# Kernel optimization log

Measured on AMD Instinct MI355X. Metric: run time of the kernel, lower is better.

Reference implementation:

```python
import jax, jax.numpy as jnp
import numpy as np

# Constants from the torch module
S_DECAY = 0.95    # sentence_decay
P_DECAY = 0.99    # paragraph_decay
D_DECAY = 0.999   # document_decay
ALPHA = 0.1       # delta_update alpha for sentence/paragraph
DOC_ALPHA = 0.05  # delta_update alpha for document
BETA = 1.0
PARA_GROUP = 5    # sentences per paragraph
EPS = 1e-12       # F.normalize eps


def _normalize(x):
    # matches torch.nn.functional.normalize(x, dim=-1)
    return x / jnp.maximum(jnp.linalg.norm(x, axis=-1, keepdims=True), EPS)


def _delta_step(M, kn, v, alpha, beta):
    # M: [H, dk, dv]; kn: [dk] (already L2-normalized); v: [dv]
    # M_new = M @ (I - alpha * kn kn^T) + beta * kn v^T   (erase matrix is symmetric,
    # so the einsum 'hkv,hkj->hjv' form equals this rank-1 update -- no dk x dk matrix needed)
    kTM = jnp.einsum('k,hkv->hv', kn, M)                       # [H, dv]
    return M - alpha * kn[None, :, None] * kTM[:, None, :] \
             + beta * (kn[:, None] * v[None, :])[None, :, :]


def _scan_updates(M0, K, V, decay, alpha, beta):
    # Streaming delta-rule: per step, decay then erase/write.
    def step(M, kv):
        k, v = kv
        M = M * decay
        M = _delta_step(M, _normalize(k), v, alpha, beta)
        return M, None
    M, _ = jax.lax.scan(step, M0, (K, V))
    return M


def setup_inputs() -> dict:
    key = jax.random.key(0)
    ks = jax.random.split(key, 7)
    T, d_emb, d_k, d_v, H = 1000, 768, 256, 256, 8
    emb = jax.random.normal(ks[0], (T, d_emb), dtype=jnp.float32)
    q = jax.random.normal(ks[1], (d_k,), dtype=jnp.float32)
    W_k = jax.random.normal(ks[2], (d_emb, d_k), dtype=jnp.float32) * 0.02
    b_k = jax.random.normal(ks[3], (d_k,), dtype=jnp.float32) * 0.02
    W_v = jax.random.normal(ks[4], (d_emb, d_v), dtype=jnp.float32) * 0.02
    b_v = jax.random.normal(ks[5], (d_v,), dtype=jnp.float32) * 0.02
    M_sent0 = jnp.zeros((H, d_k, d_v), dtype=jnp.float32)
    M_para0 = jnp.zeros((H, d_k, d_v), dtype=jnp.float32)
    M_doc0 = jnp.zeros((H, d_k, d_v), dtype=jnp.float32)
    return {"emb": emb, "q": q, "W_k": W_k, "b_k": b_k, "W_v": W_v, "b_v": b_v,
            "M_sent0": M_sent0, "M_para0": M_para0, "M_doc0": M_doc0}


def reference(emb, q, W_k, b_k, W_v, b_v, M_sent0, M_para0, M_doc0):
    T, d_emb = emb.shape
    # Level 1: sentence memory -- one delta update per sentence embedding
    K = emb @ W_k + b_k            # [T, dk]
    V = emb @ W_v + b_v            # [T, dv]
    M_sent = _scan_updates(M_sent0, K, V, S_DECAY, ALPHA, BETA)
    # Level 2: paragraph memory -- mean of each group of 5 sentence embeddings
    para_emb = emb.reshape(T // PARA_GROUP, PARA_GROUP, d_emb).mean(axis=1)
    PK = para_emb @ W_k + b_k
    PV = para_emb @ W_v + b_v
    M_para = _scan_updates(M_para0, PK, PV, P_DECAY, ALPHA, BETA)
    # Level 3: document memory -- single update from paragraph-memory statistics
    doc_k = M_para.mean(axis=0).mean(axis=-1)   # [dk]
    doc_v = M_para.mean(axis=0).mean(axis=0)    # [dv]
    M_doc = M_doc0 * D_DECAY
    M_doc = _delta_step(M_doc, _normalize(doc_k), doc_v, DOC_ALPHA, BETA)
    # recall(q, level='all')
    qn = _normalize(q)
    def recall(M):
        return jnp.einsum('hkv,k->hv', M, qn).mean(axis=0)   # [dv]
    return 0.2 * recall(M_sent) + 0.3 * recall(M_para) + 0.5 * recall(M_doc)
```

## Files before the change

### kernel.cpp

```cpp
#include <hip/hip_runtime.h>
#include <hip/hip_bf16.h>

#define ALPHA   0.1f
#define S_DECAY 0.95f
#define P_DECAY 0.99f
#define D_EMB   768
#define DK      256

template<int ctrl, int row_mask>
__device__ __forceinline__ float dpp_add(float x) {
    int y = __builtin_amdgcn_update_dpp(0, __float_as_int(x), ctrl, row_mask, 0xF, true);
    return x + __int_as_float(y);
}

template<int N>
__device__ __forceinline__ void wave_allred_arr(float (&x)[N]) {
#pragma unroll
    for (int n = 0; n < N; ++n) x[n] = dpp_add<0xB1,  0xF>(x[n]);
#pragma unroll
    for (int n = 0; n < N; ++n) x[n] = dpp_add<0x4E,  0xF>(x[n]);
#pragma unroll
    for (int n = 0; n < N; ++n) x[n] = dpp_add<0x141, 0xF>(x[n]);
#pragma unroll
    for (int n = 0; n < N; ++n) x[n] = dpp_add<0x140, 0xF>(x[n]);
#pragma unroll
    for (int n = 0; n < N; ++n) x[n] = dpp_add<0x142, 0xA>(x[n]);
#pragma unroll
    for (int n = 0; n < N; ++n) x[n] = dpp_add<0x143, 0xC>(x[n]);
#pragma unroll
    for (int n = 0; n < N; ++n)
        x[n] = __int_as_float(__builtin_amdgcn_readlane(__float_as_int(x[n]), 63));
}

__device__ __forceinline__ float dot4v(const float4& a, const float4& b) {
    float t0 = a.x * b.x; t0 = fmaf(a.y, b.y, t0);
    float t1 = a.z * b.z; t1 = fmaf(a.w, b.w, t1);
    return t0 + t1;
}

__device__ __forceinline__ float rl(float x, int lane) {
    return __int_as_float(__builtin_amdgcn_readlane(__float_as_int(x), lane));
}

__global__ __launch_bounds__(256) void prep_kernel(
    const float* __restrict__ emb,
    const float* __restrict__ Wk, const float* __restrict__ bk,
    const float* __restrict__ Wv, const float* __restrict__ bv,
    float* __restrict__ K, float* __restrict__ V, float* __restrict__ USrev,
    float* __restrict__ out, int T)
{
    const int tid = threadIdx.x;
    const int bid = blockIdx.x;
    const int NBLK = (T / 4) * 2;
    if (bid >= NBLK) {
        const int PADS = ((T + 63) / 64) * 64;
        for (int i = tid; i < (PADS - T) * DK; i += 256) USrev[(size_t)T * DK + i] = 0.f;
        out[tid] = 0.f;
        return;
    }
    const int mat = bid & 1;
    const int r0  = (bid >> 1) * 4;

    __shared__ float se[4][D_EMB];
    __shared__ float s_red[4][4];

    const float4* emb4 = reinterpret_cast<const float4*>(emb);
#pragma unroll
    for (int r = 0; r < 4; ++r) {
        if (tid < D_EMB / 4)
            reinterpret_cast<float4*>(se[r])[tid] = emb4[(size_t)(r0 + r) * (D_EMB / 4) + tid];
    }
    __syncthreads();

    const float* Wp = mat ? Wv : Wk;
    const float* bp = mat ? bv : bk;
    const int j = tid;

    float a0 = 0.f, a1 = 0.f, a2 = 0.f, a3 = 0.f;
    float c0 = Wp[j],        c1 = Wp[j + DK],     c2 = Wp[j + 2*DK], c3 = Wp[j + 3*DK];
    float p0 = Wp[j + 4*DK], p1 = Wp[j + 5*DK],   p2 = Wp[j + 6*DK], p3 = Wp[j + 7*DK];

    for (int d = 0; d < D_EMB; d += 4) {
        int dn = d + 8; if (dn >= D_EMB) dn = 0;
        const float* wn = Wp + (size_t)dn * DK + j;
        float n0 = wn[0], n1 = wn[DK], n2 = wn[2*DK], n3 = wn[3*DK];

        float4 e0 = *reinterpret_cast<const float4*>(&se[0][d]);
        float4 e1 = *reinterpret_cast<const float4*>(&se[1][d]);
        float4 e2 = *reinterpret_cast<const float4*>(&se[2][d]);
        float4 e3 = *reinterpret_cast<const float4*>(&se[3][d]);

        a0 = fmaf(e0.x, c0, a0); a0 = fmaf(e0.y, c1, a0);
        a0 = fmaf(e0.z, c2, a0); a0 = fmaf(e0.w, c3, a0);
        a1 = fmaf(e1.x, c0, a1); a1 = fmaf(e1.y, c1, a1);
        a1 = fmaf(e1.z, c2, a1); a1 = fmaf(e1.w, c3, a1);
        a2 = fmaf(e2.x, c0, a2); a2 = fmaf(e2.y, c1, a2);
        a2 = fmaf(e2.z, c2, a2); a2 = fmaf(e2.w, c3, a2);
        a3 = fmaf(e3.x, c0, a3); a3 = fmaf(e3.y, c1, a3);
        a3 = fmaf(e3.z, c2, a3); a3 = fmaf(e3.w, c3, a3);

        c0 = p0; c1 = p1; c2 = p2; c3 = p3;
        p0 = n0; p1 = n1; p2 = n2; p3 = n3;
    }

    float bj = bp[j];
    float o0 = a0 + bj, o1 = a1 + bj, o2 = a2 + bj, o3 = a3 + bj;
    float* dst = mat ? V : K;
    dst[(size_t)(r0 + 0) * DK + j] = o0;
    dst[(size_t)(r0 + 1) * DK + j] = o1;
    dst[(size_t)(r0 + 2) * DK + j] = o2;
    dst[(size_t)(r0 + 3) * DK + j] = o3;

    if (mat == 0) {
        const int wave = tid >> 6, l = tid & 63;
        float red[4] = { o0*o0, o1*o1, o2*o2, o3*o3 };
        wave_allred_arr(red);
        if (l == 0) {
            s_red[wave][0] = red[0]; s_red[wave][1] = red[1];
            s_red[wave][2] = red[2]; s_red[wave][3] = red[3];
        }
        __syncthreads();
        float t0 = s_red[0][0] + s_red[1][0] + s_red[2][0] + s_red[3][0];
        float t1 = s_red[0][1] + s_red[1][1] + s_red[2][1] + s_red[3][1];
        float t2 = s_red[0][2] + s_red[1][2] + s_red[2][2] + s_red[3][2];
        float t3 = s_red[0][3] + s_red[1][3] + s_red[2][3] + s_red[3][3];
        USrev[(size_t)(T - 1 - (r0 + 0)) * DK + j] = o0 * (1.0f / fmaxf(sqrtf(t0), 1e-12f));
        USrev[(size_t)(T - 1 - (r0 + 1)) * DK + j] = o1 * (1.0f / fmaxf(sqrtf(t1), 1e-12f));
        USrev[(size_t)(T - 1 - (r0 + 2)) * DK + j] = o2 * (1.0f / fmaxf(sqrtf(t2), 1e-12f));
        USrev[(size_t)(T - 1 - (r0 + 3)) * DK + j] = o3 * (1.0f / fmaxf(sqrtf(t3), 1e-12f));
    }
}

#define SU_STRIDE 260
__global__ __launch_bounds__(256) void graminv_kernel(
    const float* __restrict__ K, const float* __restrict__ V,
    const float* __restrict__ USrev,
    float* __restrict__ UPrev, float* __restrict__ UPfwd,
    float* __restrict__ PV, float* __restrict__ SVv,
    float* __restrict__ AinvT, float* __restrict__ F1, float* __restrict__ biasF,
    int P, int NCS, int NCP)
{
    __shared__ float sU[64 * SU_STRIDE];
    __shared__ float sA[64 * 65];
    __shared__ float sX[64 * 65];
    __shared__ float s_sv[64];
    __shared__ float s_pd[64];
    __shared__ float4 s_f1w[4][64];
    const int tid = threadIdx.x, wv = tid >> 6, l = tid & 63;
    const int bid = blockIdx.x;
    int type, m;
    if (bid < NCS)            { type = 0; m = bid; }
    else if (bid < NCS + NCP) { type = 1; m = bid - NCS; }
    else                      { type = 2; m = bid - NCS - NCP; }

    if (tid < 64) s_pd[tid] = powf(P_DECAY, (float)tid);

    float4 f1p = make_float4(0.f, 0.f, 0.f, 0.f);

    if (type == 0) {
        const float4* U4 = reinterpret_cast<const float4*>(USrev) + (size_t)m * 4096;
        for (int idx = tid; idx < 4096; idx += 256) {
            float4 t = U4[idx];
            int row = idx >> 6, c4 = (idx & 63) << 2;
            *reinterpret_cast<float4*>(&sU[row * SU_STRIDE + c4]) = t;
        }
    } else if (type == 1) {
        const float4* K4 = reinterpret_cast<const float4*>(K);
        for (int ii = 0; ii < 16; ++ii) {
            int i = wv * 16 + ii;
            int p = P - 1 - (64 * m + i);
            float4 u = make_float4(0.f, 0.f, 0.f, 0.f);
            if (p >= 0) {
                float4 pk = make_float4(0.f, 0.f, 0.f, 0.f);
#pragma unroll
                for (int s = 0; s < 5; ++s) {
                    float4 k4 = K4[(size_t)(5 * p + s) * 64 + l];
                    pk.x += k4.x; pk.y += k4.y; pk.z += k4.z; pk.w += k4.w;
                }
                pk.x *= 0.2f; pk.y *= 0.2f; pk.z *= 0.2f; pk.w *= 0.2f;
                float red[1] = { dot4v(pk, pk) };
                wave_allred_arr(red);
                float inv = 1.0f / fmaxf(sqrtf(red[0]), 1e-12f);
                u = make_float4(pk.x * inv, pk.y * inv, pk.z * inv, pk.w * inv);
            }
            *reinterpret_cast<float4*>(&sU[i * SU_STRIDE + 4 * l]) = u;
            reinterpret_cast<float4*>(UPrev)[(size_t)(64 * m + i) * 64 + l] = u;
        }
    } else {
        const float4* K4 = reinterpret_cast<const float4*>(K);
        const float4* V4 = reinterpret_cast<const float4*>(V);
        for (int ii = 0; ii < 16; ++ii) {
            int i = wv * 16 + ii;
            int p = 64 * m + i;
            float4 u = make_float4(0.f, 0.f, 0.f, 0.f);
            float sv = 0.f;
            if (p < P) {
                float4 pk = make_float4(0.f, 0.f, 0.f, 0.f);
                float4 pv = make_float4(0.f, 0.f, 0.f, 0.f);
#pragma unroll
                for (int s = 0; s < 5; ++s) {
                    float4 k4 = K4[(size_t)(5 * p + s) * 64 + l];
                    float4 v4 = V4[(size_t)(5 * p + s) * 64 + l];
                    pk.x += k4.x; pk.y += k4.y; pk.z += k4.z; pk.w += k4.w;
                    pv.x += v4.x; pv.y += v4.y; pv.z += v4.z; pv.w += v4.w;
                }
                pk.x *= 0.2f; pk.y *= 0.2f; pk.z *= 0.2f; pk.w *= 0.2f;
                pv.x *= 0.2f; pv.y *= 0.2f; pv.z *= 0.2f; pv.w *= 0.2f;
                reinterpret_cast<float4*>(PV)[(size_t)p * 64 + l] = pv;
                float red[2] = { dot4v(pk, pk), pv.x + pv.y + pv.z + pv.w };
                wave_allred_arr(red);
                float inv = 1.0f / fmaxf(sqrtf(red[0]), 1e-12f);
                u = make_float4(pk.x * inv, pk.y * inv, pk.z * inv, pk.w * inv);
                sv = red[1];
            }
            *reinterpret_cast<float4*>(&sU[i * SU_STRIDE + 4 * l]) = u;
            reinterpret_cast<float4*>(UPfwd)[(size_t)(64 * m + i) * 64 + l] = u;
            if (l == 0) { s_sv[i] = sv; SVv[64 * m + i] = sv; }
            float f = powf(P_DECAY, (float)(63 - i)) * sv;
            f1p.x = fmaf(f, u.x, f1p.x); f1p.y = fmaf(f, u.y, f1p.y);
            f1p.z = fmaf(f, u.z, f1p.z); f1p.w = fmaf(f, u.w, f1p.w);
        }
        s_f1w[wv][l] = f1p;
    }
    __syncthreads();

    if (type == 2 && wv == 0) {
        float4 a = s_f1w[0][l], b = s_f1w[1][l], c = s_f1w[2][l], d = s_f1w[3][l];
        float4 tot = make_float4(a.x+b.x+c.x+d.x, a.y+b.y+c.y+d.y,
                                 a.z+b.z+c.z+d.z, a.w+b.w+c.w+d.w);
        reinterpret_cast<float4*>(F1)[(size_t)m * 64 + l] = tot;
    }

    const int tr = tid & 15, tcg = tid >> 4;
    const int i0 = tr * 4, j0 = tcg * 4;
    if (tcg <= tr) {
        float g[4][4];
#pragma unroll
        for (int r = 0; r < 4; ++r)
#pragma unroll
            for (int c = 0; c < 4; ++c) g[r][c] = 0.f;
        for (int k4 = 0; k4 < 64; ++k4) {
            float4 A0 = *reinterpret_cast<const float4*>(&sU[(i0    ) * SU_STRIDE + 4*k4]);
            float4 A1 = *reinterpret_cast<const float4*>(&sU[(i0 + 1) * SU_STRIDE + 4*k4]);
            float4 A2 = *reinterpret_cast<const float4*>(&sU[(i0 + 2) * SU_STRIDE + 4*k4]);
            float4 A3 = *reinterpret_cast<const float4*>(&sU[(i0 + 3) * SU_STRIDE + 4*k4]);
            float4 B0 = *reinterpret_cast<const float4*>(&sU[(j0    ) * SU_STRIDE + 4*k4]);
            float4 B1 = *reinterpret_cast<const float4*>(&sU[(j0 + 1) * SU_STRIDE + 4*k4]);
            float4 B2 = *reinterpret_cast<const float4*>(&sU[(j0 + 2) * SU_STRIDE + 4*k4]);
            float4 B3 = *reinterpret_cast<const float4*>(&sU[(j0 + 3) * SU_STRIDE + 4*k4]);
            g[0][0] += dot4v(A0, B0); g[0][1] += dot4v(A0, B1);
            g[0][2] += dot4v(A0, B2); g[0][3] += dot4v(A0, B3);
            g[1][0] += dot4v(A1, B0); g[1][1] += dot4v(A1, B1);
            g[1][2] += dot4v(A1, B2); g[1][3] += dot4v(A1, B3);
            g[2][0] += dot4v(A2, B0); g[2][1] += dot4v(A2, B1);
            g[2][2] += dot4v(A2, B2); g[2][3] += dot4v(A2, B3);
            g[3][0] += dot4v(A3, B0); g[3][1] += dot4v(A3, B1);
            g[3][2] += dot4v(A3, B2); g[3][3] += dot4v(A3, B3);
        }
#pragma unroll
        for (int r = 0; r < 4; ++r)
#pragma unroll
            for (int c = 0; c < 4; ++c) {
                int gi = i0 + r, gj = j0 + c;
                float val = 0.f;
                if (gj < gi) {
                    val = ALPHA * g[r][c];
                    if (type == 2) val *= s_pd[gi - gj];
                }
                sA[gi * 65 + gj] = val;
            }
    } else {
#pragma unroll
        for (int r = 0; r < 4; ++r)
#pragma unroll
            for (int c = 0; c < 4; ++c)
                sA[(i0 + r) * 65 + j0 + c] = 0.f;
    }
    __syncthreads();

    if (type == 2 && wv == 0) {
        float dotb = 0.f;
#pragma unroll
        for (int jj = 0; jj < 64; ++jj)
            dotb = fmaf(sA[l * 65 + jj], s_sv[jj], dotb);
        biasF[m * 64 + l] = dotb * (1.0f / ALPHA);
    }

    {
        const int base = wv * 16;
        float x[16];
#pragma unroll
        for (int r = 0; r < 16; ++r) x[r] = (base + r == l) ? 1.f : 0.f;
        for (int s = 0; s < 4; ++s) {
            if (wv == s) {
#pragma unroll
                for (int i = 1; i < 16; ++i)
#pragma unroll
                    for (int jj = 0; jj < 16; ++jj)
                        if (jj < i)
                            x[i] = fmaf(-sA[(base + i) * 65 + (base + jj)], x[jj], x[i]);
#pragma unroll
                for (int r = 0; r < 16; ++r) sX[(base + r) * 65 + l] = x[r];
            }
            __syncthreads();
            if (wv > s) {
#pragma unroll
                for (int i = 0; i < 16; ++i) {
                    float xi = sX[(s * 16 + i) * 65 + l];
#pragma unroll
                    for (int r = 0; r < 16; ++r)
                        x[r] = fmaf(-sA[(base + r) * 65 + (s * 16 + i)], xi, x[r]);
                }
            }
        }
    }
    __syncthreads();

    float* dstA = AinvT + (size_t)bid * 4096;
    for (int idx = tid; idx < 4096; idx += 256) {
        int jcol = idx >> 6, irow = idx & 63;
        dstA[idx] = sX[irow * 65 + jcol];
    }
}

__global__ __launch_bounds__(512) void solve_kernel(
    const float* __restrict__ USrev, const float* __restrict__ UPrev,
    const float* __restrict__ UPfwd, const float* __restrict__ AinvT,
    const float* __restrict__ F1, const float* __restrict__ biasF,
    const float* __restrict__ q,
    float* __restrict__ BS, float* __restrict__ BPB1, float* __restrict__ BPB2,
    float* __restrict__ gscal, int NCS, int NCP)
{
    __shared__ float s_cp[8][64], s_cp2[8][64];
    __shared__ float4 s_part[8][64], s_part2[8][64];
    __shared__ float s_powd[65];
    const int tid = threadIdx.x, wave = tid >> 6, l = tid & 63;
    const int wb = wave * 8;
    if (tid <= 64) s_powd[tid] = powf(P_DECAY, (float)tid);

    float4 q4 = reinterpret_cast<const float4*>(q)[l];
    float qs[1] = { dot4v(q4, q4) };
    wave_allred_arr(qs);
    float qinv = 1.0f / fmaxf(sqrtf(qs[0]), 1e-12f);
    float4 qn = make_float4(q4.x * qinv, q4.y * qinv, q4.z * qinv, q4.w * qinv);
    __syncthreads();

    if (blockIdx.x == 0) {
        float4 w1 = qn;
        const float4* U4 = reinterpret_cast<const float4*>(USrev);
        float4 curU[8]; float curX[8];
#pragma unroll
        for (int r = 0; r < 8; ++r) {
            curU[r] = U4[(size_t)(wb + r) * 64 + l];
            curX[r] = AinvT[(size_t)(wb + r) * 64 + l];
        }
        for (int m = 0; m < NCS; ++m) {
            float4 nxtU[8]; float nxtX[8];
            if (m + 1 < NCS) {
#pragma unroll
                for (int r = 0; r < 8; ++r) {
                    nxtU[r] = U4[(size_t)(m + 1) * 4096 + (size_t)(wb + r) * 64 + l];
                    nxtX[r] = AinvT[(size_t)(m + 1) * 4096 + (size_t)(wb + r) * 64 + l];
                }
            }
            float d[8];
#pragma unroll
            for (int r = 0; r < 8; ++r) d[r] = dot4v(curU[r], w1);
            wave_allred_arr(d);
            if (l == 0) {
#pragma unroll
                for (int r = 0; r < 8; ++r) BS[m * 64 + wb + r] = d[r];
            }
            float cp = 0.f;
#pragma unroll
            for (int r = 0; r < 8; ++r) cp = fmaf(curX[r], d[r], cp);
            s_cp[wave][l] = cp;
            __syncthreads();
            float cl = 0.f;
#pragma unroll
            for (int w = 0; w < 8; ++w) cl += s_cp[w][l];
            float4 part = make_float4(0.f, 0.f, 0.f, 0.f);
#pragma unroll
            for (int r = 0; r < 8; ++r) {
                float ci = rl(cl, wb + r);
                part.x = fmaf(ci, curU[r].x, part.x); part.y = fmaf(ci, curU[r].y, part.y);
                part.z = fmaf(ci, curU[r].z, part.z); part.w = fmaf(ci, curU[r].w, part.w);
            }
            s_part[wave][l] = part;
            __syncthreads();
            float4 s = make_float4(0.f, 0.f, 0.f, 0.f);
#pragma unroll
            for (int w = 0; w < 8; ++w) {
                float4 p = s_part[w][l];
                s.x += p.x; s.y += p.y; s.z += p.z; s.w += p.w;
            }
            w1.x = fmaf(-ALPHA, s.x, w1.x); w1.y = fmaf(-ALPHA, s.y, w1.y);
            w1.z = fmaf(-ALPHA, s.z, w1.z); w1.w = fmaf(-ALPHA, s.w, w1.w);
            if (m + 1 < NCS) {
#pragma unroll
                for (int r = 0; r < 8; ++r) { curU[r] = nxtU[r]; curX[r] = nxtX[r]; }
            }
        }
    } else {
        {
            float4 w1 = qn;
            float4 w2 = make_float4(1.f, 1.f, 1.f, 1.f);
            const float4* U4 = reinterpret_cast<const float4*>(UPrev);
            float4 curU[8]; float curX[8];
#pragma unroll
            for (int r = 0; r < 8; ++r) {
                curU[r] = U4[(size_t)(wb + r) * 64 + l];
                curX[r] = AinvT[(size_t)NCS * 4096 + (size_t)(wb + r) * 64 + l];
            }
            for (int m = 0; m < NCP; ++m) {
                float4 nxtU[8]; float nxtX[8];
                if (m + 1 < NCP) {
#pragma unroll
                    for (int r = 0; r < 8; ++r) {
                        nxtU[r] = U4[(size_t)(m + 1) * 4096 + (size_t)(wb + r) * 64 + l];
                        nxtX[r] = AinvT[(size_t)(NCS + m + 1) * 4096 + (size_t)(wb + r) * 64 + l];
                    }
                }
                float d[16];
#pragma unroll
                for (int r = 0; r < 8; ++r) {
                    d[r]     = dot4v(curU[r], w1);
                    d[8 + r] = dot4v(curU[r], w2);
                }
                wave_allred_arr(d);
                if (l == 0) {
#pragma unroll
                    for (int r = 0; r < 8; ++r) {
                        BPB1[m * 64 + wb + r] = d[r];
                        BPB2[m * 64 + wb + r] = d[8 + r];
                    }
                }
                float cp1 = 0.f, cp2 = 0.f;
#pragma unroll
                for (int r = 0; r < 8; ++r) {
                    cp1 = fmaf(curX[r], d[r], cp1);
                    cp2 = fmaf(curX[r], d[8 + r], cp2);
                }
                s_cp[wave][l] = cp1; s_cp2[wave][l] = cp2;
                __syncthreads();
                float cl1 = 0.f, cl2 = 0.f;
#pragma unroll
                for (int w = 0; w < 8; ++w) { cl1 += s_cp[w][l]; cl2 += s_cp2[w][l]; }
                float4 p1 = make_float4(0.f,0.f,0.f,0.f), p2 = make_float4(0.f,0.f,0.f,0.f);
#pragma unroll
                for (int r = 0; r < 8; ++r) {
                    float c1 = rl(cl1, wb + r), c2 = rl(cl2, wb + r);
                    p1.x = fmaf(c1, curU[r].x, p1.x); p1.y = fmaf(c1, curU[r].y, p1.y);
                    p1.z = fmaf(c1, curU[r].z, p1.z); p1.w = fmaf(c1, curU[r].w, p1.w);
                    p2.x = fmaf(c2, curU[r].x, p2.x); p2.y = fmaf(c2, curU[r].y, p2.y);
                    p2.z = fmaf(c2, curU[r].z, p2.z); p2.w = fmaf(c2, curU[r].w, p2.w);
                }
                s_part[wave][l] = p1; s_part2[wave][l] = p2;
                __syncthreads();
                float4 s1 = make_float4(0.f,0.f,0.f,0.f), s2 = make_float4(0.f,0.f,0.f,0.f);
#pragma unroll
                for (int w = 0; w < 8; ++w) {
                    float4 a = s_part[w][l];  float4 b = s_part2[w][l];
                    s1.x += a.x; s1.y += a.y; s1.z += a.z; s1.w += a.w;
                    s2.x += b.x; s2.y += b.y; s2.z += b.z; s2.w += b.w;
                }
                w1.x = fmaf(-ALPHA, s1.x, w1.x); w1.y = fmaf(-ALPHA, s1.y, w1.y);
                w1.z = fmaf(-ALPHA, s1.z, w1.z); w1.w = fmaf(-ALPHA, s1.w, w1.w);
                w2.x = fmaf(-ALPHA, s2.x, w2.x); w2.y = fmaf(-ALPHA, s2.y, w2.y);
                w2.z = fmaf(-ALPHA, s2.z, w2.z); w2.w = fmaf(-ALPHA, s2.w, w2.w);
                if (m + 1 < NCP) {
#pragma unroll
                    for (int r = 0; r < 8; ++r) { curU[r] = nxtU[r]; curX[r] = nxtX[r]; }
                }
            }
        }
        __syncthreads();
        float4 y = make_float4(0.f, 0.f, 0.f, 0.f);
        {
            const float4* U4 = reinterpret_cast<const float4*>(UPfwd);
            float4 curU[8]; float curX[8];
#pragma unroll
            for (int r = 0; r < 8; ++r) {
                curU[r] = U4[(size_t)(wb + r) * 64 + l];
                curX[r] = AinvT[(size_t)(NCS + NCP) * 4096 + (size_t)(wb + r) * 64 + l];
            }
            for (int m = 0; m < NCP; ++m) {
                float4 nxtU[8]; float nxtX[8];
                if (m + 1 < NCP) {
#pragma unroll
                    for (int r = 0; r < 8; ++r) {
                        nxtU[r] = U4[(size_t)(m + 1) * 4096 + (size_t)(wb + r) * 64 + l];
                        nxtX[r] = AinvT[(size_t)(NCS + NCP + m + 1) * 4096 + (size_t)(wb + r) * 64 + l];
                    }
                }
                float biasr[8];
#pragma unroll
                for (int r = 0; r < 8; ++r) biasr[r] = biasF[m * 64 + wb + r];
                float4 f1 = reinterpret_cast<const float4*>(F1)[(size_t)m * 64 + l];
                float d[8];
#pragma unroll
                for (int r = 0; r < 8; ++r) d[r] = dot4v(curU[r], y);
                wave_allred_arr(d);
#pragma unroll
                for (int r = 0; r < 8; ++r)
                    d[r] = fmaf(s_powd[wb + r + 1], d[r], biasr[r]);
                float cp = 0.f;
#pragma unroll
                for (int r = 0; r < 8; ++r) cp = fmaf(curX[r], d[r], cp);
                s_cp[wave][l] = cp;
                __syncthreads();
                float cl = 0.f;
#pragma unroll
                for (int w = 0; w < 8; ++w) cl += s_cp[w][l];
                float4 part = make_float4(0.f, 0.f, 0.f, 0.f);
#pragma unroll
                for (int r = 0; r < 8; ++r) {
                    float ci = s_powd[63 - (wb + r)] * rl(cl, wb + r);
                    part.x = fmaf(ci, curU[r].x, part.x); part.y = fmaf(ci, curU[r].y, part.y);
                    part.z = fmaf(ci, curU[r].z, part.z); part.w = fmaf(ci, curU[r].w, part.w);
                }
                s_part[wave][l] = part;
                __syncthreads();
                float4 s = make_float4(0.f, 0.f, 0.f, 0.f);
#pragma unroll
                for (int w = 0; w < 8; ++w) {
                    float4 p = s_part[w][l];
                    s.x += p.x; s.y += p.y; s.z += p.z; s.w += p.w;
                }
                float d64 = s_powd[64];
                y.x = fmaf(d64, y.x, fmaf(-ALPHA, s.x, f1.x));
                y.y = fmaf(d64, y.y, fmaf(-ALPHA, s.y, f1.y));
                y.z = fmaf(d64, y.z, fmaf(-ALPHA, s.z, f1.z));
                y.w = fmaf(d64, y.w, fmaf(-ALPHA, s.w, f1.w));
                if (m + 1 < NCP) {
#pragma unroll
                    for (int r = 0; r < 8; ++r) { curU[r] = nxtU[r]; curX[r] = nxtX[r]; }
                }
            }
        }
        float fin[2] = { dot4v(y, y), dot4v(qn, y) };
        wave_allred_arr(fin);
        if (tid == 0) gscal[0] = fin[1] / fmaxf(sqrtf(fin[0]), 2.56e-10f);
    }
}

__global__ __launch_bounds__(256) void accum_kernel(
    const float* __restrict__ V, const float* __restrict__ PV,
    const float* __restrict__ AinvT,
    const float* __restrict__ BS, const float* __restrict__ BPB1,
    const float* __restrict__ BPB2, const float* __restrict__ gscal,
    float* __restrict__ out, int T, int P, int NCS, int NCP)
{
    __shared__ float s_b[64], s_cp[4][64], wc[64];
    const int b = blockIdx.x, t = threadIdx.x;
    const float* src; const float* B; int i0, realN, chunk, ci; float decay;
    if (b < NCS)            { src = V;  B = BS;   ci = b;             realN = T; decay = S_DECAY; chunk = b; }
    else if (b < NCS + NCP) { src = PV; B = BPB1; ci = b - NCS;       realN = P; decay = P_DECAY; chunk = b; }
    else                    { src = PV; B = BPB2; ci = b - NCS - NCP; realN = P; decay = P_DECAY; chunk = b - NCP; }
    i0 = ci * 64;
    if (t < 64) s_b[t] = B[ci * 64 + t];
    __syncthreads();
    {
        const int part = t >> 6, k = t & 63;
        const float* Xc = AinvT + (size_t)chunk * 4096;
        float cp = 0.f;
#pragma unroll
        for (int jj = 0; jj < 16; ++jj) {
            int j = part * 16 + jj;
            cp = fmaf(Xc[j * 64 + k], s_b[j], cp);
        }
        s_cp[part][k] = cp;
    }
    __syncthreads();
    if (t < 64) {
        float c = s_cp[0][t] + s_cp[1][t] + s_cp[2][t] + s_cp[3][t];
        wc[t] = powf(decay, (float)(i0 + t)) * c;
    }
    __syncthreads();
    const int k = t;
    float acc = 0.f;
    for (int ii = 0; ii < 64; ++ii) {
        int i = i0 + ii;
        if (i < realN)
            acc = fmaf(wc[ii], src[(size_t)(realN - 1 - i) * DK + k], acc);
    }
    float wlev;
    if (b < NCS)            wlev = 0.2f;
    else if (b < NCS + NCP) wlev = 0.3f;
    else                    wlev = (0.5f / 256.0f) * gscal[0];
    atomicAdd(&out[k], wlev * acc);
}

extern "C" void kernel_launch(void* const* d_in, const int* in_sizes, int n_in,
                              void* d_out, int out_size, void* d_ws, size_t ws_size,
                              hipStream_t stream) {
    const float* emb = (const float*)d_in[0];
    const float* q   = (const float*)d_in[1];
    const float* Wk  = (const float*)d_in[2];
    const float* bk  = (const float*)d_in[3];
    const float* Wv  = (const float*)d_in[4];
    const float* bv  = (const float*)d_in[5];

    const int T = in_sizes[0] / D_EMB;
    const int P = T / 5;
    const int NCS  = (T + 63) / 64;
    const int NCP  = (P + 63) / 64;
    const int PADS = NCS * 64;
    const int PADP = NCP * 64;
    const int NCH  = NCS + 2 * NCP;

    float* ws    = (float*)d_ws;
    float* K     = ws;
    float* V     = K     + (size_t)T * DK;
    float* PV    = V     + (size_t)T * DK;
    float* USrev = PV    + (size_t)PADP * DK;
    float* UPrev = USrev + (size_t)PADS * DK;
    float* UPfwd = UPrev + (size_t)PADP * DK;
    float* SVv   = UPfwd + (size_t)PADP * DK;
    float* AinvT = SVv   + PADP;
    float* F1    = AinvT + (size_t)NCH * 4096;
    float* biasF = F1    + (size_t)NCP * 256;
    float* BS    = biasF + PADP;
    float* BPB1  = BS    + PADS;
    float* BPB2  = BPB1  + PADP;
    float* gscal = BPB2  + PADP;

    prep_kernel<<<(T / 4) * 2 + 1, 256, 0, stream>>>(emb, Wk, bk, Wv, bv,
                                                     K, V, USrev, (float*)d_out, T);
    graminv_kernel<<<NCH, 256, 0, stream>>>(K, V, USrev, UPrev, UPfwd,
                                            PV, SVv, AinvT, F1, biasF, P, NCS, NCP);
    solve_kernel<<<2, 512, 0, stream>>>(USrev, UPrev, UPfwd, AinvT, F1, biasF, q,
                                        BS, BPB1, BPB2, gscal, NCS, NCP);
    accum_kernel<<<NCH, 256, 0, stream>>>(V, PV, AinvT, BS, BPB1, BPB2, gscal,
                                          (float*)d_out, T, P, NCS, NCP);
}
```

Baseline: 186.0 us.

## Fuse four kernels into one cooperative persistent kernel with grid syncs

Merges the prep, gram-inverse, solve and accumulate kernels into a single cooperative kernel launched with 256 blocks, separated by grid.sync barriers. The prep stage becomes a grid-stride loop over its former 501 blocks, and shared memory is one buffer reused across stages. This removes three kernel-launch gaps and inter-kernel idle time. In exchange the prep stage runs on only 256 blocks, the solve stage leaves most blocks idle at a grid barrier, and the large shared allocation limits occupancy.

```diff
diff --git a/kernel.cpp b/kernel.cpp
--- a/kernel.cpp
+++ b/kernel.cpp
@@ -1,5 +1,8 @@
 #include <hip/hip_runtime.h>
 #include <hip/hip_bf16.h>
+#include <hip/hip_cooperative_groups.h>
+
+namespace cg = cooperative_groups;
 
 #define ALPHA   0.1f
 #define S_DECAY 0.95f
@@ -42,553 +45,547 @@
     return __int_as_float(__builtin_amdgcn_readlane(__float_as_int(x), lane));
 }
 
-__global__ __launch_bounds__(256) void prep_kernel(
-    const float* __restrict__ emb,
+#define SU_STRIDE 260
+#define SMEM_FLOATS 26112
+
+__global__ __launch_bounds__(256) void mega_kernel(
+    const float* __restrict__ emb, const float* __restrict__ q,
     const float* __restrict__ Wk, const float* __restrict__ bk,
     const float* __restrict__ Wv, const float* __restrict__ bv,
-    float* __restrict__ K, float* __restrict__ V, float* __restrict__ USrev,
-    float* __restrict__ out, int T)
+    float* __restrict__ K, float* __restrict__ V, float* __restrict__ PV,
+    float* __restrict__ USrev, float* __restrict__ UPrev, float* __restrict__ UPfwd,
+    float* __restrict__ SVv, float* __restrict__ AinvT, float* __restrict__ F1,
+    float* __restrict__ biasF, float* __restrict__ BS, float* __restrict__ BPB1,
+    float* __restrict__ BPB2, float* __restrict__ gscal, float* __restrict__ out,
+    int T, int P, int NCS, int NCP)
 {
+    __shared__ __align__(16) float smem[SMEM_FLOATS];
+    cg::grid_group grid = cg::this_grid();
     const int tid = threadIdx.x;
     const int bid = blockIdx.x;
-    const int NBLK = (T / 4) * 2;
-    if (bid >= NBLK) {
-        const int PADS = ((T + 63) / 64) * 64;
-        for (int i = tid; i < (PADS - T) * DK; i += 256) USrev[(size_t)T * DK + i] = 0.f;
-        out[tid] = 0.f;
-        return;
+    const int wave = tid >> 6, l = tid & 63;
+
+    {
+        float* se    = smem;
+        float* s_red = smem + 3072;
+        const int NBLK = (T / 4) * 2;
+        for (int unit = bid; unit <= NBLK; unit += gridDim.x) {
+            if (unit == NBLK) {
+                const int PADS = ((T + 63) / 64) * 64;
+                for (int i = tid; i < (PADS - T) * DK; i += 256) USrev[(size_t)T * DK + i] = 0.f;
+                out[tid] = 0.f;
+                continue;
+            }
+            const int mat = unit & 1;
+            const int r0  = (unit >> 1) * 4;
+
+            const float4* emb4 = reinterpret_cast<const float4*>(emb);
+#pragma unroll
+            for (int r = 0; r < 4; ++r) {
+                if (tid < D_EMB / 4)
+                    reinterpret_cast<float4*>(&se[r * D_EMB])[tid] =
+                        emb4[(size_t)(r0 + r) * (D_EMB / 4) + tid];
+            }
+            __syncthreads();
+
+            const float* Wp = mat ? Wv : Wk;
+            const float* bp = mat ? bv : bk;
+            const int j = tid;
+
+            float a0 = 0.f, a1 = 0.f, a2 = 0.f, a3 = 0.f;
+            float c0 = Wp[j],        c1 = Wp[j + DK],   c2 = Wp[j + 2*DK], c3 = Wp[j + 3*DK];
+            float p0 = Wp[j + 4*DK], p1 = Wp[j + 5*DK], p2 = Wp[j + 6*DK], p3 = Wp[j + 7*DK];
+
+            for (int d = 0; d < D_EMB; d += 4) {
+                int dn = d + 8; if (dn >= D_EMB) dn = 0;
+                const float* wn = Wp + (size_t)dn * DK + j;
+                float n0 = wn[0], n1 = wn[DK], n2 = wn[2*DK], n3 = wn[3*DK];
+
+                float4 e0 = *reinterpret_cast<const float4*>(&se[0 * D_EMB + d]);
+                float4 e1 = *reinterpret_cast<const float4*>(&se[1 * D_EMB + d]);
+                float4 e2 = *reinterpret_cast<const float4*>(&se[2 * D_EMB + d]);
+                float4 e3 = *reinterpret_cast<const float4*>(&se[3 * D_EMB + d]);
+
+                a0 = fmaf(e0.x, c0, a0); a0 = fmaf(e0.y, c1, a0);
+                a0 = fmaf(e0.z, c2, a0); a0 = fmaf(e0.w, c3, a0);
+                a1 = fmaf(e1.x, c0, a1); a1 = fmaf(e1.y, c1, a1);
+                a1 = fmaf(e1.z, c2, a1); a1 = fmaf(e1.w, c3, a1);
+                a2 = fmaf(e2.x, c0, a2); a2 = fmaf(e2.y, c1, a2);
+                a2 = fmaf(e2.z, c2, a2); a2 = fmaf(e2.w, c3, a2);
+                a3 = fmaf(e3.x, c0, a3); a3 = fmaf(e3.y, c1, a3);
+                a3 = fmaf(e3.z, c2, a3); a3 = fmaf(e3.w, c3, a3);
+
+                c0 = p0; c1 = p1; c2 = p2; c3 = p3;
+                p0 = n0; p1 = n1; p2 = n2; p3 = n3;
+            }
+
+            float bj = bp[j];
+            float o0 = a0 + bj, o1 = a1 + bj, o2 = a2 + bj, o3 = a3 + bj;
+            float* dst = mat ? V : K;
+            dst[(size_t)(r0 + 0) * DK + j] = o0;
+            dst[(size_t)(r0 + 1) * DK + j] = o1;
+            dst[(size_t)(r0 + 2) * DK + j] = o2;
+            dst[(size_t)(r0 + 3) * DK + j] = o3;
+
+            if (mat == 0) {
+                float red[4] = { o0*o0, o1*o1, o2*o2, o3*o3 };
+                wave_allred_arr(red);
+                if (l == 0) {
+#pragma unroll
+                    for (int n = 0; n < 4; ++n) s_red[wave * 4 + n] = red[n];
+                }
+                __syncthreads();
+                float t0 = s_red[0] + s_red[4] + s_red[8]  + s_red[12];
+                float t1 = s_red[1] + s_red[5] + s_red[9]  + s_red[13];
+                float t2 = s_red[2] + s_red[6] + s_red[10] + s_red[14];
+                float t3 = s_red[3] + s_red[7] + s_red[11] + s_red[15];
+                USrev[(size_t)(T - 1 - (r0 + 0)) * DK + j] = o0 * (1.0f / fmaxf(sqrtf(t0), 1e-12f));
+                USrev[(size_t)(T - 1 - (r0 + 1)) * DK + j] = o1 * (1.0f / fmaxf(sqrtf(t1), 1e-12f));
+                USrev[(size_t)(T - 1 - (r0 + 2)) * DK + j] = o2 * (1.0f / fmaxf(sqrtf(t2), 1e-12f));
+                USrev[(size_t)(T - 1 - (r0 + 3)) * DK + j] = o3 * (1.0f / fmaxf(sqrtf(t3), 1e-12f));
+            } else {
+                __syncthreads();
+            }
+        }
     }
-    const int mat = bid & 1;
-    const int r0  = (bid >> 1) * 4;
-
-    __shared__ float se[4][D_EMB];
-    __shared__ float s_red[4][4];
-
-    const float4* emb4 = reinterpret_cast<const float4*>(emb);
-#pragma unroll
-    for (int r = 0; r < 4; ++r) {
-        if (tid < D_EMB / 4)
-            reinterpret_cast<float4*>(se[r])[tid] = emb4[(size_t)(r0 + r) * (D_EMB / 4) + tid];
+    grid.sync();
+
+    if (bid < NCS + 2 * NCP) {
+        float*  sU    = smem;
+        float*  sA    = smem + 16640;
+        float*  sX    = smem + 20800;
+        float*  s_sv  = smem + 24960;
+        float*  s_pd  = smem + 25024;
+        float4* s_f1w = reinterpret_cast<float4*>(smem + 25088);
+
+        int type, m;
+        if (bid < NCS)            { type = 0; m = bid; }
+        else if (bid < NCS + NCP) { type = 1; m = bid - NCS; }
+        else                      { type = 2; m = bid - NCS - NCP; }
+
+        if (tid < 64) s_pd[tid] = powf(P_DECAY, (float)tid);
+
+        float4 f1p = make_float4(0.f, 0.f, 0.f, 0.f);
+
+        if (type == 0) {
+            const float4* U4 = reinterpret_cast<const float4*>(USrev) + (size_t)m * 4096;
+            for (int idx = tid; idx < 4096; idx += 256) {
+                float4 t = U4[idx];
+                int row = idx >> 6, c4 = (idx & 63) << 2;
+                *reinterpret_cast<float4*>(&sU[row * SU_STRIDE + c4]) = t;
+            }
+        } else if (type == 1) {
+            const float4* K4 = reinterpret_cast<const float4*>(K);
+            for (int ii = 0; ii < 16; ++ii) {
+                int i = wave * 16 + ii;
+                int p = P - 1 - (64 * m + i);
+                float4 u = make_float4(0.f, 0.f, 0.f, 0.f);
+                if (p >= 0) {
+                    float4 pk = make_float4(0.f, 0.f, 0.f, 0.f);
+#pragma unroll
+                    for (int s = 0; s < 5; ++s) {
+                        float4 k4 = K4[(size_t)(5 * p + s) * 64 + l];
+                        pk.x += k4.x; pk.y += k4.y; pk.z += k4.z; pk.w += k4.w;
+                    }
+                    pk.x *= 0.2f; pk.y *= 0.2f; pk.z *= 0.2f; pk.w *= 0.2f;
+                    float red[1] = { dot4v(pk, pk) };
+                    wave_allred_arr(red);
+                    float inv = 1.0f / fmaxf(sqrtf(red[0]), 1e-12f);
+                    u = make_float4(pk.x * inv, pk.y * inv, pk.z * inv, pk.w * inv);
+                }
+                *reinterpret_cast<float4*>(&sU[i * SU_STRIDE + 4 * l]) = u;
+                reinterpret_cast<float4*>(UPrev)[(size_t)(64 * m + i) * 64 + l] = u;
+            }
+        } else {
+            const float4* K4 = reinterpret_cast<const float4*>(K);
+            const float4* V4 = reinterpret_cast<const float4*>(V);
+            for (int ii = 0; ii < 16; ++ii) {
+                int i = wave * 16 + ii;
+                int p = 64 * m + i;
+                float4 u = make_float4(0.f, 0.f, 0.f, 0.f);
+                float sv = 0.f;
+                if (p < P) {
+                    float4 pk = make_float4(0.f, 0.f, 0.f, 0.f);
+                    float4 pv = make_float4(0.f, 0.f, 0.f, 0.f);
+#pragma unroll
+                    for (int s = 0; s < 5; ++s) {
+                        float4 k4 = K4[(size_t)(5 * p + s) * 64 + l];
+                        float4 v4 = V4[(size_t)(5 * p + s) * 64 + l];
+                        pk.x += k4.x; pk.y += k4.y; pk.z += k4.z; pk.w += k4.w;
+                        pv.x += v4.x; pv.y += v4.y; pv.z += v4.z; pv.w += v4.w;
+                    }
+                    pk.x *= 0.2f; pk.y *= 0.2f; pk.z *= 0.2f; pk.w *= 0.2f;
+                    pv.x *= 0.2f; pv.y *= 0.2f; pv.z *= 0.2f; pv.w *= 0.2f;
+                    reinterpret_cast<float4*>(PV)[(size_t)p * 64 + l] = pv;
+                    float red[2] = { dot4v(pk, pk), pv.x + pv.y + pv.z + pv.w };
+                    wave_allred_arr(red);
+                    float inv = 1.0f / fmaxf(sqrtf(red[0]), 1e-12f);
+                    u = make_float4(pk.x * inv, pk.y * inv, pk.z * inv, pk.w * inv);
+                    sv = red[1];
+                }
+                *reinterpret_cast<float4*>(&sU[i * SU_STRIDE + 4 * l]) = u;
+                reinterpret_cast<float4*>(UPfwd)[(size_t)(64 * m + i) * 64 + l] = u;
+                if (l == 0) { s_sv[i] = sv; SVv[64 * m + i] = sv; }
+                float f = powf(P_DECAY, (float)(63 - i)) * sv;
+                f1p.x = fmaf(f, u.x, f1p.x); f1p.y = fmaf(f, u.y, f1p.y);
+                f1p.z = fmaf(f, u.z, f1p.z); f1p.w = fmaf(f, u.w, f1p.w);
+            }
+            s_f1w[wave * 64 + l] = f1p;
+        }
+        __syncthreads();
+
+        if (type == 2 && wave == 0) {
+            float4 a = s_f1w[l], b = s_f1w[64 + l], c = s_f1w[128 + l], d = s_f1w[192 + l];
+            float4 tot = make_float4(a.x+b.x+c.x+d.x, a.y+b.y+c.y+d.y,
+                                     a.z+b.z+c.z+d.z, a.w+b.w+c.w+d.w);
+            reinterpret_cast<float4*>(F1)[(size_t)m * 64 + l] = tot;
+        }
+
+        if (tid < 136) {
+            int tr = (int)((sqrtf(8.f * (float)tid + 1.f) - 1.f) * 0.5f);
+            while ((tr + 1) * (tr + 2) / 2 <= tid) ++tr;
+            while (tr * (tr + 1) / 2 > tid) --tr;
+            int tcg = tid - tr * (tr + 1) / 2;
+            const int i0 = tr * 4, j0 = tcg * 4;
+            float g[4][4];
+#pragma unroll
+            for (int r = 0; r < 4; ++r)
+#pragma unroll
+                for (int c = 0; c < 4; ++c) g[r][c] = 0.f;
+            for (int k4 = 0; k4 < 64; ++k4) {
+                float4 A0 = *reinterpret_cast<const float4*>(&sU[(i0    ) * SU_STRIDE + 4*k4]);
+                float4 A1 = *reinterpret_cast<const float4*>(&sU[(i0 + 1) * SU_STRIDE + 4*k4]);
+                float4 A2 = *reinterpret_cast<const float4*>(&sU[(i0 + 2) * SU_STRIDE + 4*k4]);
+                float4 A3 = *reinterpret_cast<const float4*>(&sU[(i0 + 3) * SU_STRIDE + 4*k4]);
+                float4 B0 = *reinterpret_cast<const float4*>(&sU[(j0    ) * SU_STRIDE + 4*k4]);
+                float4 B1 = *reinterpret_cast<const float4*>(&sU[(j0 + 1) * SU_STRIDE + 4*k4]);
+                float4 B2 = *reinterpret_cast<const float4*>(&sU[(j0 + 2) * SU_STRIDE + 4*k4]);
+                float4 B3 = *reinterpret_cast<const float4*>(&sU[(j0 + 3) * SU_STRIDE + 4*k4]);
+                g[0][0] += dot4v(A0, B0); g[0][1] += dot4v(A0, B1);
+                g[0][2] += dot4v(A0, B2); g[0][3] += dot4v(A0, B3);
+                g[1][0] += dot4v(A1, B0); g[1][1] += dot4v(A1, B1);
+                g[1][2] += dot4v(A1, B2); g[1][3] += dot4v(A1, B3);
+                g[2][0] += dot4v(A2, B0); g[2][1] += dot4v(A2, B1);
+                g[2][2] += dot4v(A2, B2); g[2][3] += dot4v(A2, B3);
+                g[3][0] += dot4v(A3, B0); g[3][1] += dot4v(A3, B1);
+                g[3][2] += dot4v(A3, B2); g[3][3] += dot4v(A3, B3);
+            }
+#pragma unroll
+            for (int r = 0; r < 4; ++r)
+#pragma unroll
+                for (int c = 0; c < 4; ++c) {
+                    int gi = i0 + r, gj = j0 + c;
+                    float val = 0.f;
+                    if (gj < gi) {
+                        val = ALPHA * g[r][c];
+                        if (type == 2) val *= s_pd[gi - gj];
+                    }
+                    sA[gi * 65 + gj] = val;
+                }
+            if (tr != tcg) {
+#pragma unroll
+                for (int r = 0; r < 4; ++r)
+#pragma unroll
+                    for (int c = 0; c < 4; ++c)
+                        sA[(j0 + r) * 65 + i0 + c] = 0.f;
+            }
+        }
+        __syncthreads();
+
+        if (type == 2 && wave == 0) {
+            float dotb = 0.f;
+#pragma unroll
+            for (int jj = 0; jj < 64; ++jj)
+                dotb = fmaf(sA[l * 65 + jj], s_sv[jj], dotb);
+            biasF[m * 64 + l] = dotb * (1.0f / ALPHA);
+        }
+
+        {
+            const int base = wave * 16;
+            float x[16];
+#pragma unroll
+            for (int r = 0; r < 16; ++r) x[r] = (base + r == l) ? 1.f : 0.f;
+            for (int s = 0; s < 4; ++s) {
+                if (wave == s) {
+#pragma unroll
+                    for (int i = 1; i < 16; ++i)
+#pragma unroll
+                        for (int jj = 0; jj < 16; ++jj)
+                            if (jj < i)
+                                x[i] = fmaf(-sA[(base + i) * 65 + (base + jj)], x[jj], x[i]);
+#pragma unroll
+                    for (int r = 0; r < 16; ++r) sX[(base + r) * 65 + l] = x[r];
+                }
+                __syncthreads();
+                if (wave > s) {
+#pragma unroll
+                    for (int i = 0; i < 16; ++i) {
+                        float xi = sX[(s * 16 + i) * 65 + l];
+#pragma unroll
+                        for (int r = 0; r < 16; ++r)
+                            x[r] = fmaf(-sA[(base + r) * 65 + (s * 16 + i)], xi, x[r]);
+                    }
+                }
+            }
+        }
+        __syncthreads();
+
+        float* dstA = AinvT + (size_t)bid * 4096;
+        for (int idx = tid; idx < 4096; idx += 256) {
+            int jcol = idx >> 6, irow = idx & 63;
+            dstA[idx] = sX[irow * 65 + jcol];
+        }
     }
-    __syncthreads();
-
-    const float* Wp = mat ? Wv : Wk;
-    const float* bp = mat ? bv : bk;
-    const int j = tid;
-
-    float a0 = 0.f, a1 = 0.f, a2 = 0.f, a3 = 0.f;
-    float c0 = Wp[j],        c1 = Wp[j + DK],     c2 = Wp[j + 2*DK], c3 = Wp[j + 3*DK];
-    float p0 = Wp[j + 4*DK], p1 = Wp[j + 5*DK],   p2 = Wp[j + 6*DK], p3 = Wp[j + 7*DK];
-
-    for (int d = 0; d < D_EMB; d += 4) {
-        int dn = d + 8; if (dn >= D_EMB) dn = 0;
-        const float* wn = Wp + (size_t)dn * DK + j;
-        float n0 = wn[0], n1 = wn[DK], n2 = wn[2*DK], n3 = wn[3*DK];
-
-        float4 e0 = *reinterpret_cast<const float4*>(&se[0][d]);
-        float4 e1 = *reinterpret_cast<const float4*>(&se[1][d]);
-        float4 e2 = *reinterpret_cast<const float4*>(&se[2][d]);
-        float4 e3 = *reinterpret_cast<const float4*>(&se[3][d]);
-
-        a0 = fmaf(e0.x, c0, a0); a0 = fmaf(e0.y, c1, a0);
-        a0 = fmaf(e0.z, c2, a0); a0 = fmaf(e0.w, c3, a0);
-        a1 = fmaf(e1.x, c0, a1); a1 = fmaf(e1.y, c1, a1);
-        a1 = fmaf(e1.z, c2, a1); a1 = fmaf(e1.w, c3, a1);
-        a2 = fmaf(e2.x, c0, a2); a2 = fmaf(e2.y, c1, a2);
-        a2 = fmaf(e2.z, c2, a2); a2 = fmaf(e2.w, c3, a2);
-        a3 = fmaf(e3.x, c0, a3); a3 = fmaf(e3.y, c1, a3);
-        a3 = fmaf(e3.z, c2, a3); a3 = fmaf(e3.w, c3, a3);
-
-        c0 = p0; c1 = p1; c2 = p2; c3 = p3;
-        p0 = n0; p1 = n1; p2 = n2; p3 = n3;
-    }
-
-    float bj = bp[j];
-    float o0 = a0 + bj, o1 = a1 + bj, o2 = a2 + bj, o3 = a3 + bj;
-    float* dst = mat ? V : K;
-    dst[(size_t)(r0 + 0) * DK + j] = o0;
-    dst[(size_t)(r0 + 1) * DK + j] = o1;
-    dst[(size_t)(r0 + 2) * DK + j] = o2;
-    dst[(size_t)(r0 + 3) * DK + j] = o3;
-
-    if (mat == 0) {
-        const int wave = tid >> 6, l = tid & 63;
-        float red[4] = { o0*o0, o1*o1, o2*o2, o3*o3 };
-        wave_allred_arr(red);
-        if (l == 0) {
-            s_red[wave][0] = red[0]; s_red[wave][1] = red[1];
-            s_red[wave][2] = red[2]; s_red[wave][3] = red[3];
-        }
+    grid.sync();
+
+    if (bid < 2) {
+        float*  s_cp   = smem;
+        float*  s_cp2  = smem + 256;
+        float4* s_part  = reinterpret_cast<float4*>(smem + 512);
+        float4* s_part2 = reinterpret_cast<float4*>(smem + 1536);
+        float*  s_powd = smem + 2560;
+        const int wb = wave * 16;
+        if (tid <= 64) s_powd[tid] = powf(P_DECAY, (float)tid);
+
+        float4 q4 = reinterpret_cast<const float4*>(q)[l];
+        float qs[1] = { dot4v(q4, q4) };
+        wave_allred_arr(qs);
+        float qinv = 1.0f / fmaxf(sqrtf(qs[0]), 1e-12f);
+        float4 qn = make_float4(q4.x * qinv, q4.y * qinv, q4.z * qinv, q4.w * qinv);
         __syncthreads();
-        float t0 = s_red[0][0] + s_red[1][0] + s_red[2][0] + s_red[3][0];
-        float t1 = s_red[0][1] + s_red[1][1] + s_red[2][1] + s_red[3][1];
-        float t2 = s_red[0][2] + s_red[1][2] + s_red[2][2] + s_red[3][2];
-        float t3 = s_red[0][3] + s_red[1][3] + s_red[2][3] + s_red[3][3];
-        USrev[(size_t)(T - 1 - (r0 + 0)) * DK + j] = o0 * (1.0f / fmaxf(sqrtf(t0), 1e-12f));
-        USrev[(size_t)(T - 1 - (r0 + 1)) * DK + j] = o1 * (1.0f / fmaxf(sqrtf(t1), 1e-12f));
-        USrev[(size_t)(T - 1 - (r0 + 2)) * DK + j] = o2 * (1.0f / fmaxf(sqrtf(t2), 1e-12f));
-        USrev[(size_t)(T - 1 - (r0 + 3)) * DK + j] = o3 * (1.0f / fmaxf(sqrtf(t3), 1e-12f));
-    }
-}
-
-#define SU_STRIDE 260
-__global__ __launch_bounds__(256) void graminv_kernel(
-    const float* __restrict__ K, const float* __restrict__ V,
-    const float* __restrict__ USrev,
-    float* __restrict__ UPrev, float* __restrict__ UPfwd,
-    float* __restrict__ PV, float* __restrict__ SVv,
-    float* __restrict__ AinvT, float* __restrict__ F1, float* __restrict__ biasF,
-    int P, int NCS, int NCP)
-{
-    __shared__ float sU[64 * SU_STRIDE];
-    __shared__ float sA[64 * 65];
-    __shared__ float sX[64 * 65];
-    __shared__ float s_sv[64];
-    __shared__ float s_pd[64];
-    __shared__ float4 s_f1w[4][64];
-    const int tid = threadIdx.x, wv = tid >> 6, l = tid & 63;
-    const int bid = blockIdx.x;
-    int type, m;
-    if (bid < NCS)            { type = 0; m = bid; }
-    else if (bid < NCS + NCP) { type = 1; m = bid - NCS; }
-    else                      { type = 2; m = bid - NCS - NCP; }
-
-    if (tid < 64) s_pd[tid] = powf(P_DECAY, (float)tid);
-
-    float4 f1p = make_float4(0.f, 0.f, 0.f, 0.f);
-
-    if (type == 0) {
-        const float4* U4 = reinterpret_cast<const float4*>(USrev) + (size_t)m * 4096;
-        for (int idx = tid; idx < 4096; idx += 256) {
-            float4 t = U4[idx];
-            int row = idx >> 6, c4 = (idx & 63) << 2;
-            *reinterpret_cast<float4*>(&sU[row * SU_STRIDE + c4]) = t;
-        }
-    } else if (type == 1) {
-        const float4* K4 = reinterpret_cast<const float4*>(K);
-        for (int ii = 0; ii < 16; ++ii) {
-            int i = wv * 16 + ii;
-            int p = P - 1 - (64 * m + i);
-            float4 u = make_float4(0.f, 0.f, 0.f, 0.f);
-            if (p >= 0) {
-                float4 pk = make_float4(0.f, 0.f, 0.f, 0.f);
-#pragma unroll
-                for (int s = 0; s < 5; ++s) {
-                    float4 k4 = K4[(size_t)(5 * p + s) * 64 + l];
-                    pk.x += k4.x; pk.y += k4.y; pk.z += k4.z; pk.w += k4.w;
-                }
-                pk.x *= 0.2f; pk.y *= 0.2f; pk.z *= 0.2f; pk.w *= 0.2f;
-                float red[1] = { dot4v(pk, pk) };
-                wave_allred_arr(red);
-                float inv = 1.0f / fmaxf(sqrtf(red[0]), 1e-12f);
-                u = make_float4(pk.x * inv, pk.y * inv, pk.z * inv, pk.w * inv);
-            }
-            *reinterpret_cast<float4*>(&sU[i * SU_STRIDE + 4 * l]) = u;
-            reinterpret_cast<float4*>(UPrev)[(size_t)(64 * m + i) * 64 + l] = u;
-        }
-    } else {
-        const float4* K4 = reinterpret_cast<const float4*>(K);
-        const float4* V4 = reinterpret_cast<const float4*>(V);
-        for (int ii = 0; ii < 16; ++ii) {
-            int i = wv * 16 + ii;
-            int p = 64 * m + i;
-            float4 u = make_float4(0.f, 0.f, 0.f, 0.f);
-            float sv = 0.f;
-            if (p < P) {
-                float4 pk = make_float4(0.f, 0.f, 0.f, 0.f);
-                float4 pv = make_float4(0.f, 0.f, 0.f, 0.f);
-#pragma unroll
-                for (int s = 0; s < 5; ++s) {
-                    float4 k4 = K4[(size_t)(5 * p + s) * 64 + l];
-                    float4 v4 = V4[(size_t)(5 * p + s) * 64 + l];
-                    pk.x += k4.x; pk.y += k4.y; pk.z += k4.z; pk.w += k4.w;
-                    pv.x += v4.x; pv.y += v4.y; pv.z += v4.z; pv.w += v4.w;
-                }
-                pk.x *= 0.2f; pk.y *= 0.2f; pk.z *= 0.2f; pk.w *= 0.2f;
-                pv.x *= 0.2f; pv.y *= 0.2f; pv.z *= 0.2f; pv.w *= 0.2f;
-                reinterpret_cast<float4*>(PV)[(size_t)p * 64 + l] = pv;
-                float red[2] = { dot4v(pk, pk), pv.x + pv.y + pv.z + pv.w };
-                wave_allred_arr(red);
-                float inv = 1.0f / fmaxf(sqrtf(red[0]), 1e-12f);
-                u = make_float4(pk.x * inv, pk.y * inv, pk.z * inv, pk.w * inv);
-                sv = red[1];
-            }
-            *reinterpret_cast<float4*>(&sU[i * SU_STRIDE + 4 * l]) = u;
-            reinterpret_cast<float4*>(UPfwd)[(size_t)(64 * m + i) * 64 + l] = u;
-            if (l == 0) { s_sv[i] = sv; SVv[64 * m + i] = sv; }
-            float f = powf(P_DECAY, (float)(63 - i)) * sv;
-            f1p.x = fmaf(f, u.x, f1p.x); f1p.y = fmaf(f, u.y, f1p.y);
-            f1p.z = fmaf(f, u.z, f1p.z); f1p.w = fmaf(f, u.w, f1p.w);
-        }
-        s_f1w[wv][l] = f1p;
-    }
-    __syncthreads();
-
-    if (type == 2 && wv == 0) {
-        float4 a = s_f1w[0][l], b = s_f1w[1][l], c = s_f1w[2][l], d = s_f1w[3][l];
-        float4 tot = make_float4(a.x+b.x+c.x+d.x, a.y+b.y+c.y+d.y,
-                                 a.z+b.z+c.z+d.z, a.w+b.w+c.w+d.w);
-        reinterpret_cast<float4*>(F1)[(size_t)m * 64 + l] = tot;
-    }
-
-    const int tr = tid & 15, tcg = tid >> 4;
-    const int i0 = tr * 4, j0 = tcg * 4;
-    if (tcg <= tr) {
-        float g[4][4];
-#pragma unroll
-        for (int r = 0; r < 4; ++r)
-#pragma unroll
-            for (int c = 0; c < 4; ++c) g[r][c] = 0.f;
-        for (int k4 = 0; k4 < 64; ++k4) {
-            float4 A0 = *reinterpret_cast<const float4*>(&sU[(i0    ) * SU_STRIDE + 4*k4]);
-            float4 A1 = *reinterpret_cast<const float4*>(&sU[(i0 + 1) * SU_STRIDE + 4*k4]);
-            float4 A2 = *reinterpret_cast<const float4*>(&sU[(i0 + 2) * SU_STRIDE + 4*k4]);
-            float4 A3 = *reinterpret_cast<const float4*>(&sU[(i0 + 3) * SU_STRIDE + 4*k4]);
-            float4 B0 = *reinterpret_cast<const float4*>(&sU[(j0    ) * SU_STRIDE + 4*k4]);
-            float4 B1 = *reinterpret_cast<const float4*>(&sU[(j0 + 1) * SU_STRIDE + 4*k4]);
-            float4 B2 = *reinterpret_cast<const float4*>(&sU[(j0 + 2) * SU_STRIDE + 4*k4]);
-            float4 B3 = *reinterpret_cast<const float4*>(&sU[(j0 + 3) * SU_STRIDE + 4*k4]);
-            g[0][0] += dot4v(A0, B0); g[0][1] += dot4v(A0, B1);
-            g[0][2] += dot4v(A0, B2); g[0][3] += dot4v(A0, B3);
-            g[1][0] += dot4v(A1, B0); g[1][1] += dot4v(A1, B1);
-            g[1][2] += dot4v(A1, B2); g[1][3] += dot4v(A1, B3);
-            g[2][0] += dot4v(A2, B0); g[2][1] += dot4v(A2, B1);
-            g[2][2] += dot4v(A2, B2); g[2][3] += dot4v(A2, B3);
-            g[3][0] += dot4v(A3, B0); g[3][1] += dot4v(A3, B1);
-            g[3][2] += dot4v(A3, B2); g[3][3] += dot4v(A3, B3);
-        }
-#pragma unroll
-        for (int r = 0; r < 4; ++r)
-#pragma unroll
-            for (int c = 0; c < 4; ++c) {
-                int gi = i0 + r, gj = j0 + c;
-                float val = 0.f;
-                if (gj < gi) {
-                    val = ALPHA * g[r][c];
-                    if (type == 2) val *= s_pd[gi - gj];
-                }
-                sA[gi * 65 + gj] = val;
-            }
-    } else {
-#pragma unroll
-        for (int r = 0; r < 4; ++r)
-#pragma unroll
-            for (int c = 0; c < 4; ++c)
-                sA[(i0 + r) * 65 + j0 + c] = 0.f;
-    }
-    __syncthreads();
-
-    if (type == 2 && wv == 0) {
-        float dotb = 0.f;
-#pragma unroll
-        for (int jj = 0; jj < 64; ++jj)
-            dotb = fmaf(sA[l * 65 + jj], s_sv[jj], dotb);
-        biasF[m * 64 + l] = dotb * (1.0f / ALPHA);
-    }
-
-    {
-        const int base = wv * 16;
-        float x[16];
-#pragma unroll
-        for (int r = 0; r < 16; ++r) x[r] = (base + r == l) ? 1.f : 0.f;
-        for (int s = 0; s < 4; ++s) {
-            if (wv == s) {
-#pragma unroll
-                for (int i = 1; i < 16; ++i)
-#pragma unroll
-                    for (int jj = 0; jj < 16; ++jj)
-                        if (jj < i)
-                            x[i] = fmaf(-sA[(base + i) * 65 + (base + jj)], x[jj], x[i]);
-#pragma unroll
-                for (int r = 0; r < 16; ++r) sX[(base + r) * 65 + l] = x[r];
-            }
-            __syncthreads();
-            if (wv > s) {
-#pragma unroll
-                for (int i = 0; i < 16; ++i) {
-                    float xi = sX[(s * 16 + i) * 65 + l];
-#pragma unroll
-                    for (int r = 0; r < 16; ++r)
-                        x[r] = fmaf(-sA[(base + r) * 65 + (s * 16 + i)], xi, x[r]);
-                }
-            }
-        }
-    }
-    __syncthreads();
-
-    float* dstA = AinvT + (size_t)bid * 4096;
-    for (int idx = tid; idx < 4096; idx += 256) {
-        int jcol = idx >> 6, irow = idx & 63;
-        dstA[idx] = sX[irow * 65 + jcol];
-    }
-}
-
-__global__ __launch_bounds__(512) void solve_kernel(
-    const float* __restrict__ USrev, const float* __restrict__ UPrev,
-    const float* __restrict__ UPfwd, const float* __restrict__ AinvT,
-    const float* __restrict__ F1, const float* __restrict__ biasF,
-    const float* __restrict__ q,
-    float* __restrict__ BS, float* __restrict__ BPB1, float* __restrict__ BPB2,
-    float* __restrict__ gscal, int NCS, int NCP)
-{
-    __shared__ float s_cp[8][64], s_cp2[8][64];
-    __shared__ float4 s_part[8][64], s_part2[8][64];
-    __shared__ float s_powd[65];
-    const int tid = threadIdx.x, wave = tid >> 6, l = tid & 63;
-    const int wb = wave * 8;
-    if (tid <= 64) s_powd[tid] = powf(P_DECAY, (float)tid);
-
-    float4 q4 = reinterpret_cast<const float4*>(q)[l];
-    float qs[1] = { dot4v(q4, q4) };
-    wave_allred_arr(qs);
-    float qinv = 1.0f / fmaxf(sqrtf(qs[0]), 1e-12f);
-    float4 qn = make_float4(q4.x * qinv, q4.y * qinv, q4.z * qinv, q4.w * qinv);
-    __syncthreads();
-
-    if (blockIdx.x == 0) {
-        float4 w1 = qn;
-        const float4* U4 = reinterpret_cast<const float4*>(USrev);
-        float4 curU[8]; float curX[8];
-#pragma unroll
-        for (int r = 0; r < 8; ++r) {
-            curU[r] = U4[(size_t)(wb + r) * 64 + l];
-            curX[r] = AinvT[(size_t)(wb + r) * 64 + l];
-        }
-        for (int m = 0; m < NCS; ++m) {
-            float4 nxtU[8]; float nxtX[8];
-            if (m + 1 < NCS) {
-#pragma unroll
-                for (int r = 0; r < 8; ++r) {
-                    nxtU[r] = U4[(size_t)(m + 1) * 4096 + (size_t)(wb + r) * 64 + l];
-                    nxtX[r] = AinvT[(size_t)(m + 1) * 4096 + (size_t)(wb + r) * 64 + l];
-                }
-            }
-            float d[8];
-#pragma unroll
-            for (int r = 0; r < 8; ++r) d[r] = dot4v(curU[r], w1);
-            wave_allred_arr(d);
-            if (l == 0) {
-#pragma unroll
-                for (int r = 0; r < 8; ++r) BS[m * 64 + wb + r] = d[r];
-            }
-            float cp = 0.f;
-#pragma unroll
-            for (int r = 0; r < 8; ++r) cp = fmaf(curX[r], d[r], cp);
-            s_cp[wave][l] = cp;
-            __syncthreads();
-            float cl = 0.f;
-#pragma unroll
-            for (int w = 0; w < 8; ++w) cl += s_cp[w][l];
-            float4 part = make_float4(0.f, 0.f, 0.f, 0.f);
-#pragma unroll
-            for (int r = 0; r < 8; ++r) {
-                float ci = rl(cl, wb + r);
-                part.x = fmaf(ci, curU[r].x, part.x); part.y = fmaf(ci, curU[r].y, part.y);
-                part.z = fmaf(ci, curU[r].z, part.z); part.w = fmaf(ci, curU[r].w, part.w);
-            }
-            s_part[wave][l] = part;
-            __syncthreads();
-            float4 s = make_float4(0.f, 0.f, 0.f, 0.f);
-#pragma unroll
-            for (int w = 0; w < 8; ++w) {
-                float4 p = s_part[w][l];
-                s.x += p.x; s.y += p.y; s.z += p.z; s.w += p.w;
-            }
-            w1.x = fmaf(-ALPHA, s.x, w1.x); w1.y = fmaf(-ALPHA, s.y, w1.y);
-            w1.z = fmaf(-ALPHA, s.z, w1.z); w1.w = fmaf(-ALPHA, s.w, w1.w);
-            if (m + 1 < NCS) {
-#pragma unroll
-                for (int r = 0; r < 8; ++r) { curU[r] = nxtU[r]; curX[r] = nxtX[r]; }
-            }
-        }
-    } else {
-        {
+
+        if (bid == 0) {
             float4 w1 = qn;
-            float4 w2 = make_float4(1.f, 1.f, 1.f, 1.f);
-            const float4* U4 = reinterpret_cast<const float4*>(UPrev);
-            float4 curU[8]; float curX[8];
-#pragma unroll
-            for (int r = 0; r < 8; ++r) {
+            const float4* U4 = reinterpret_cast<const float4*>(USrev);
+            float4 curU[16]; float curX[16];
+#pragma unroll
+            for (int r = 0; r < 16; ++r) {
                 curU[r] = U4[(size_t)(wb + r) * 64 + l];
-                curX[r] = AinvT[(size_t)NCS * 4096 + (size_t)(wb + r) * 64 + l];
-            }
-            for (int m = 0; m < NCP; ++m) {
-                float4 nxtU[8]; float nxtX[8];
-                if (m + 1 < NCP) {
-#pragma unroll
-                    for (int r = 0; r < 8; ++r) {
+                curX[r] = AinvT[(size_t)(wb + r) * 64 + l];
+            }
+            for (int m = 0; m < NCS; ++m) {
+                float4 nxtU[16]; float nxtX[16];
+                if (m + 1 < NCS) {
+#pragma unroll
+                    for (int r = 0; r < 16; ++r) {
                         nxtU[r] = U4[(size_t)(m + 1) * 4096 + (size_t)(wb + r) * 64 + l];
-                        nxtX[r] = AinvT[(size_t)(NCS + m + 1) * 4096 + (size_t)(wb + r) * 64 + l];
+                        nxtX[r] = AinvT[(size_t)(m + 1) * 4096 + (size_t)(wb + r) * 64 + l];
                     }
                 }
                 float d[16];
 #pragma unroll
-                for (int r = 0; r < 8; ++r) {
-                    d[r]     = dot4v(curU[r], w1);
-                    d[8 + r] = dot4v(curU[r], w2);
-                }
+                for (int r = 0; r < 16; ++r) d[r] = dot4v(curU[r], w1);
                 wave_allred_arr(d);
                 if (l == 0) {
 #pragma unroll
-                    for (int r = 0; r < 8; ++r) {
-                        BPB1[m * 64 + wb + r] = d[r];
-                        BPB2[m * 64 + wb + r] = d[8 + r];
-                    }
-                }
-                float cp1 = 0.f, cp2 = 0.f;
-#pragma unroll
-                for (int r = 0; r < 8; ++r) {
-                    cp1 = fmaf(curX[r], d[r], cp1);
-                    cp2 = fmaf(curX[r], d[8 + r], cp2);
-                }
-                s_cp[wave][l] = cp1; s_cp2[wave][l] = cp2;
+                    for (int r = 0; r < 16; ++r) BS[m * 64 + wb + r] = d[r];
+                }
+                float cp = 0.f;
+#pragma unroll
+                for (int r = 0; r < 16; ++r) cp = fmaf(curX[r], d[r], cp);
+                s_cp[wave * 64 + l] = cp;
                 __syncthreads();
-                float cl1 = 0.f, cl2 = 0.f;
-#pragma unroll
-                for (int w = 0; w < 8; ++w) { cl1 += s_cp[w][l]; cl2 += s_cp2[w][l]; }
-                float4 p1 = make_float4(0.f,0.f,0.f,0.f), p2 = make_float4(0.f,0.f,0.f,0.f);
-#pragma unroll
-                for (int r = 0; r < 8; ++r) {
-                    float c1 = rl(cl1, wb + r), c2 = rl(cl2, wb + r);
-                    p1.x = fmaf(c1, curU[r].x, p1.x); p1.y = fmaf(c1, curU[r].y, p1.y);
-                    p1.z = fmaf(c1, curU[r].z, p1.z); p1.w = fmaf(c1, curU[r].w, p1.w);
-                    p2.x = fmaf(c2, curU[r].x, p2.x); p2.y = fmaf(c2, curU[r].y, p2.y);
-                    p2.z = fmaf(c2, curU[r].z, p2.z); p2.w = fmaf(c2, curU[r].w, p2.w);
-                }
-                s_part[wave][l] = p1; s_part2[wave][l] = p2;
-                __syncthreads();
-                float4 s1 = make_float4(0.f,0.f,0.f,0.f), s2 = make_float4(0.f,0.f,0.f,0.f);
-#pragma unroll
-                for (int w = 0; w < 8; ++w) {
-                    float4 a = s_part[w][l];  float4 b = s_part2[w][l];
-                    s1.x += a.x; s1.y += a.y; s1.z += a.z; s1.w += a.w;
-                    s2.x += b.x; s2.y += b.y; s2.z += b.z; s2.w += b.w;
-                }
-                w1.x = fmaf(-ALPHA, s1.x, w1.x); w1.y = fmaf(-ALPHA, s1.y, w1.y);
-                w1.z = fmaf(-ALPHA, s1.z, w1.z); w1.w = fmaf(-ALPHA, s1.w, w1.w);
-                w2.x = fmaf(-ALPHA, s2.x, w2.x); w2.y = fmaf(-ALPHA, s2.y, w2.y);
-                w2.z = fmaf(-ALPHA, s2.z, w2.z); w2.w = fmaf(-ALPHA, s2.w, w2.w);
-                if (m + 1 < NCP) {
-#pragma unroll
-                    for (int r = 0; r < 8; ++r) { curU[r] = nxtU[r]; curX[r] = nxtX[r]; }
-                }
-            }
-        }
-        __syncthreads();
-        float4 y = make_float4(0.f, 0.f, 0.f, 0.f);
-        {
-            const float4* U4 = reinterpret_cast<const float4*>(UPfwd);
-            float4 curU[8]; float curX[8];
-#pragma unroll
-            for (int r = 0; r < 8; ++r) {
-                curU[r] = U4[(size_t)(wb + r) * 64 + l];
-                curX[r] = AinvT[(size_t)(NCS + NCP) * 4096 + (size_t)(wb + r) * 64 + l];
-            }
-            for (int m = 0; m < NCP; ++m) {
-                float4 nxtU[8]; float nxtX[8];
-                if (m + 1 < NCP) {
-#pragma unroll
-                    for (int r = 0; r < 8; ++r) {
-                        nxtU[r] = U4[(size_t)(m + 1) * 4096 + (size_t)(wb + r) * 64 + l];
-                        nxtX[r] = AinvT[(size_t)(NCS + NCP + m + 1) * 4096 + (size_t)(wb + r) * 64 + l];
-                    }
-                }
-                float biasr[8];
-#pragma unroll
-                for (int r = 0; r < 8; ++r) biasr[r] = biasF[m * 64 + wb + r];
-                float4 f1 = reinterpret_cast<const float4*>(F1)[(size_t)m * 64 + l];
-                float d[8];
-#pragma unroll
-                for (int r = 0; r < 8; ++r) d[r] = dot4v(curU[r], y);
-                wave_allred_arr(d);
-#pragma unroll
-                for (int r = 0; r < 8; ++r)
-                    d[r] = fmaf(s_powd[wb + r + 1], d[r], biasr[r]);
-                float cp = 0.f;
-#pragma unroll
-                for (int r = 0; r < 8; ++r) cp = fmaf(curX[r], d[r], cp);
-                s_cp[wave][l] = cp;
-                __syncthreads();
-                float cl = 0.f;
-#pragma unroll
-                for (int w = 0; w < 8; ++w) cl += s_cp[w][l];
+                float cl = s_cp[l] + s_cp[64 + l] + s_cp[128 + l] + s_cp[192 + l];
                 float4 part = make_float4(0.f, 0.f, 0.f, 0.f);
 #pragma unroll
-                for (int r = 0; r < 8; ++r) {
-                    float ci = s_powd[63 - (wb + r)] * rl(cl, wb + r);
+                for (int r = 0; r < 16; ++r) {
+                    float ci = rl(cl, wb + r);
                     part.x = fmaf(ci, curU[r].x, part.x); part.y = fmaf(ci, curU[r].y, part.y);
                     part.z = fmaf(ci, curU[r].z, part.z); part.w = fmaf(ci, curU[r].w, part.w);
                 }
-                s_part[wave][l] = part;
+                s_part[wave * 64 + l] = part;
                 __syncthreads();
-                float4 s = make_float4(0.f, 0.f, 0.f, 0.f);
-#pragma unroll
-                for (int w = 0; w < 8; ++w) {
-                    float4 p = s_part[w][l];
-                    s.x += p.x; s.y += p.y; s.z += p.z; s.w += p.w;
-                }
-                float d64 = s_powd[64];
-                y.x = fmaf(d64, y.x, fmaf(-ALPHA, s.x, f1.x));
-                y.y = fmaf(d64, y.y, fmaf(-ALPHA, s.y, f1.y));
-                y.z = fmaf(d64, y.z, fmaf(-ALPHA, s.z, f1.z));
-                y.w = fmaf(d64, y.w, fmaf(-ALPHA, s.w, f1.w));
-                if (m + 1 < NCP) {
-#pragma unroll
-                    for (int r = 0; r < 8; ++r) { curU[r] = nxtU[r]; curX[r] = nxtX[r]; }
-                }
-            }
-        }
-        float fin[2] = { dot4v(y, y), dot4v(qn, y) };
-        wave_allred_arr(fin);
-        if (tid == 0) gscal[0] = fin[1] / fmaxf(sqrtf(fin[0]), 2.56e-10f);
+                float4 p0 = s_part[l], p1 = s_part[64 + l], p2 = s_part[128 + l], p3 = s_part[192 + l];
+                float4 s = make_float4(p0.x+p1.x+p2.x+p3.x, p0.y+p1.y+p2.y+p3.y,
+                                       p0.z+p1.z+p2.z+p3.z, p0.w+p1.w+p2.w+p3.w);
+                w1.x = fmaf(-ALPHA, s.x, w1.x); w1.y = fmaf(-ALPHA, s.y, w1.y);
+                w1.z = fmaf(-ALPHA, s.z, w1.z); w1.w = fmaf(-ALPHA, s.w, w1.w);
+                if (m + 1 < NCS) {
+#pragma unroll
+                    for (int r = 0; r < 16; ++r) { curU[r] = nxtU[r]; curX[r] = nxtX[r]; }
+                }
+            }
+        } else {
+            {
+                float4 w1 = qn;
+                float4 w2 = make_float4(1.f, 1.f, 1.f, 1.f);
+                const float4* U4 = reinterpret_cast<const float4*>(UPrev);
+                float4 curU[16]; float curX[16];
+#pragma unroll
+                for (int r = 0; r < 16; ++r) {
+                    curU[r] = U4[(size_t)(wb + r) * 64 + l];
+                    curX[r] = AinvT[(size_t)NCS * 4096 + (size_t)(wb + r) * 64 + l];
+                }
+                for (int m = 0; m < NCP; ++m) {
+                    float4 nxtU[16]; float nxtX[16];
+                    if (m + 1 < NCP) {
+#pragma unroll
+                        for (int r = 0; r < 16; ++r) {
+                            nxtU[r] = U4[(size_t)(m + 1) * 4096 + (size_t)(wb + r) * 64 + l];
+                            nxtX[r] = AinvT[(size_t)(NCS + m + 1) * 4096 + (size_t)(wb + r) * 64 + l];
+                        }
+                    }
+                    float d[32];
+#pragma unroll
+                    for (int r = 0; r < 16; ++r) {
+                        d[r]      = dot4v(curU[r], w1);
+                        d[16 + r] = dot4v(curU[r], w2);
+                    }
+                    wave_allred_arr(d);
+                    if (l == 0) {
+#pragma unroll
+                        for (int r = 0; r < 16; ++r) {
+                            BPB1[m * 64 + wb + r] = d[r];
+                            BPB2[m * 64 + wb + r] = d[16 + r];
+                        }
+                    }
+                    float cp1 = 0.f, cp2 = 0.f;
+#pragma unroll
+                    for (int r = 0; r < 16; ++r) {
+                        cp1 = fmaf(curX[r], d[r], cp1);
+                        cp2 = fmaf(curX[r], d[16 + r], cp2);
+                    }
+                    s_cp[wave * 64 + l] = cp1; s_cp2[wave * 64 + l] = cp2;
+                    __syncthreads();
+                    float cl1 = s_cp[l] + s_cp[64 + l] + s_cp[128 + l] + s_cp[192 + l];
+                    float cl2 = s_cp2[l] + s_cp2[64 + l] + s_cp2[128 + l] + s_cp2[192 + l];
+                    float4 p1 = make_float4(0.f,0.f,0.f,0.f), p2v = make_float4(0.f,0.f,0.f,0.f);
+#pragma unroll
+                    for (int r = 0; r < 16; ++r) {
+                        float c1 = rl(cl1, wb + r), c2 = rl(cl2, wb + r);
+                        p1.x = fmaf(c1, curU[r].x, p1.x); p1.y = fmaf(c1, curU[r].y, p1.y);
+                        p1.z = fmaf(c1, curU[r].z, p1.z); p1.w = fmaf(c1, curU[r].w, p1.w);
+                        p2v.x = fmaf(c2, curU[r].x, p2v.x); p2v.y = fmaf(c2, curU[r].y, p2v.y);
+                        p2v.z = fmaf(c2, curU[r].z, p2v.z); p2v.w = fmaf(c2, curU[r].w, p2v.w);
+                    }
+                    s_part[wave * 64 + l] = p1; s_part2[wave * 64 + l] = p2v;
+                    __syncthreads();
+                    {
+                        float4 a0 = s_part[l], a1 = s_part[64+l], a2 = s_part[128+l], a3 = s_part[192+l];
+                        float4 b0 = s_part2[l], b1 = s_part2[64+l], b2 = s_part2[128+l], b3 = s_part2[192+l];
+                        w1.x = fmaf(-ALPHA, a0.x+a1.x+a2.x+a3.x, w1.x);
+                        w1.y = fmaf(-ALPHA, a0.y+a1.y+a2.y+a3.y, w1.y);
+                        w1.z = fmaf(-ALPHA, a0.z+a1.z+a2.z+a3.z, w1.z);
+                        w1.w = fmaf(-ALPHA, a0.w+a1.w+a2.w+a3.w, w1.w);
+                        w2.x = fmaf(-ALPHA, b0.x+b1.x+b2.x+b3.x, w2.x);
+                        w2.y = fmaf(-ALPHA, b0.y+b1.y+b2.y+b3.y, w2.y);
+                        w2.z = fmaf(-ALPHA, b0.z+b1.z+b2.z+b3.z, w2.z);
+                        w2.w = fmaf(-ALPHA, b0.w+b1.w+b2.w+b3.w, w2.w);
+                    }
+                    if (m + 1 < NCP) {
+#pragma unroll
+                        for (int r = 0; r < 16; ++r) { curU[r] = nxtU[r]; curX[r] = nxtX[r]; }
+                    }
+                }
+            }
+            __syncthreads();
+            float4 y = make_float4(0.f, 0.f, 0.f, 0.f);
+            {
+                const float4* U4 = reinterpret_cast<const float4*>(UPfwd);
+                float4 curU[16]; float curX[16];
+#pragma unroll
+                for (int r = 0; r < 16; ++r) {
+                    curU[r] = U4[(size_t)(wb + r) * 64 + l];
+                    curX[r] = AinvT[(size_t)(NCS + NCP) * 4096 + (size_t)(wb + r) * 64 + l];
+                }
+                for (int m = 0; m < NCP; ++m) {
+                    float4 nxtU[16]; float nxtX[16];
+                    if (m + 1 < NCP) {
+#pragma unroll
+                        for (int r = 0; r < 16; ++r) {
+                            nxtU[r] = U4[(size_t)(m + 1) * 4096 + (size_t)(wb + r) * 64 + l];
+                            nxtX[r] = AinvT[(size_t)(NCS + NCP + m + 1) * 4096 + (size_t)(wb + r) * 64 + l];
+                        }
+                    }
+                    float biasr[16];
+#pragma unroll
+                    for (int r = 0; r < 16; ++r) biasr[r] = biasF[m * 64 + wb + r];
+                    float4 f1 = reinterpret_cast<const float4*>(F1)[(size_t)m * 64 + l];
+                    float d[16];
+#pragma unroll
+                    for (int r = 0; r < 16; ++r) d[r] = dot4v(curU[r], y);
+                    wave_allred_arr(d);
+#pragma unroll
+                    for (int r = 0; r < 16; ++r)
+                        d[r] = fmaf(s_powd[wb + r + 1], d[r], biasr[r]);
+                    float cp = 0.f;
+#pragma unroll
+                    for (int r = 0; r < 16; ++r) cp = fmaf(curX[r], d[r], cp);
+                    s_cp[wave * 64 + l] = cp;
+                    __syncthreads();
+                    float cl = s_cp[l] + s_cp[64 + l] + s_cp[128 + l] + s_cp[192 + l];
+                    float4 part = make_float4(0.f, 0.f, 0.f, 0.f);
+#pragma unroll
+                    for (int r = 0; r < 16; ++r) {
+                        float ci = s_powd[63 - (wb + r)] * rl(cl, wb + r);
+                        part.x = fmaf(ci, curU[r].x, part.x); part.y = fmaf(ci, curU[r].y, part.y);
+                        part.z = fmaf(ci, curU[r].z, part.z); part.w = fmaf(ci, curU[r].w, part.w);
+                    }
+                    s_part[wave * 64 + l] = part;
+                    __syncthreads();
+                    float4 p0 = s_part[l], p1 = s_part[64 + l], p2 = s_part[128 + l], p3 = s_part[192 + l];
+                    float4 s = make_float4(p0.x+p1.x+p2.x+p3.x, p0.y+p1.y+p2.y+p3.y,
+                                           p0.z+p1.z+p2.z+p3.z, p0.w+p1.w+p2.w+p3.w);
+                    float d64 = s_powd[64];
+                    y.x = fmaf(d64, y.x, fmaf(-ALPHA, s.x, f1.x));
+                    y.y = fmaf(d64, y.y, fmaf(-ALPHA, s.y, f1.y));
+                    y.z = fmaf(d64, y.z, fmaf(-ALPHA, s.z, f1.z));
+                    y.w = fmaf(d64, y.w, fmaf(-ALPHA, s.w, f1.w));
+                    if (m + 1 < NCP) {
+#pragma unroll
+                        for (int r = 0; r < 16; ++r) { curU[r] = nxtU[r]; curX[r] = nxtX[r]; }
+                    }
+                }
+            }
+            float fin[2] = { dot4v(y, y), dot4v(qn, y) };
+            wave_allred_arr(fin);
+            if (tid == 0) gscal[0] = fin[1] / fmaxf(sqrtf(fin[0]), 2.56e-10f);
+        }
     }
-}
-
-__global__ __launch_bounds__(256) void accum_kernel(
-    const float* __restrict__ V, const float* __restrict__ PV,
-    const float* __restrict__ AinvT,
-    const float* __restrict__ BS, const float* __restrict__ BPB1,
-    const float* __restrict__ BPB2, const float* __restrict__ gscal,
-    float* __restrict__ out, int T, int P, int NCS, int NCP)
-{
-    __shared__ float s_b[64], s_cp[4][64], wc[64];
-    const int b = blockIdx.x, t = threadIdx.x;
-    const float* src; const float* B; int i0, realN, chunk, ci; float decay;
-    if (b < NCS)            { src = V;  B = BS;   ci = b;             realN = T; decay = S_DECAY; chunk = b; }
-    else if (b < NCS + NCP) { src = PV; B = BPB1; ci = b - NCS;       realN = P; decay = P_DECAY; chunk = b; }
-    else                    { src = PV; B = BPB2; ci = b - NCS - NCP; realN = P; decay = P_DECAY; chunk = b - NCP; }
-    i0 = ci * 64;
-    if (t < 64) s_b[t] = B[ci * 64 + t];
-    __syncthreads();
-    {
-        const int part = t >> 6, k = t & 63;
-        const float* Xc = AinvT + (size_t)chunk * 4096;
-        float cp = 0.f;
-#pragma unroll
-        for (int jj = 0; jj < 16; ++jj) {
-            int j = part * 16 + jj;
-            cp = fmaf(Xc[j * 64 + k], s_b[j], cp);
-        }
-        s_cp[part][k] = cp;
+    grid.sync();
+
+    if (bid < NCS + 2 * NCP) {
+        float* s_b  = smem;
+        float* s_cpA = smem + 64;
+        float* wc   = smem + 320;
+        const int b = bid, t = tid;
+        const float* src; const float* B; int i0, realN, chunk, ci; float decay;
+        if (b < NCS)            { src = V;  B = BS;   ci = b;             realN = T; decay = S_DECAY; chunk = b; }
+        else if (b < NCS + NCP) { src = PV; B = BPB1; ci = b - NCS;       realN = P; decay = P_DECAY; chunk = b; }
+        else                    { src = PV; B = BPB2; ci = b - NCS - NCP; realN = P; decay = P_DECAY; chunk = b - NCP; }
+        i0 = ci * 64;
+        if (t < 64) s_b[t] = B[ci * 64 + t];
+        __syncthreads();
+        {
+            const int part = t >> 6, k = t & 63;
+            const float* Xc = AinvT + (size_t)chunk * 4096;
+            float cp = 0.f;
+#pragma unroll
+            for (int jj = 0; jj < 16; ++jj) {
+                int j = part * 16 + jj;
+                cp = fmaf(Xc[j * 64 + k], s_b[j], cp);
+            }
+            s_cpA[part * 64 + k] = cp;
+        }
+        __syncthreads();
+        if (t < 64) {
+            float c = s_cpA[t] + s_cpA[64 + t] + s_cpA[128 + t] + s_cpA[192 + t];
+            wc[t] = powf(decay, (float)(i0 + t)) * c;
+        }
+        __syncthreads();
+        const int k = t;
+        float acc = 0.f;
+        for (int ii = 0; ii < 64; ++ii) {
+            int i = i0 + ii;
+            if (i < realN)
+                acc = fmaf(wc[ii], src[(size_t)(realN - 1 - i) * DK + k], acc);
+        }
+        float wlev;
+        if (b < NCS)            wlev = 0.2f;
+        else if (b < NCS + NCP) wlev = 0.3f;
+        else                    wlev = (0.5f / 256.0f) * gscal[0];
+        atomicAdd(&out[k], wlev * acc);
     }
-    __syncthreads();
-    if (t < 64) {
-        float c = s_cp[0][t] + s_cp[1][t] + s_cp[2][t] + s_cp[3][t];
-        wc[t] = powf(decay, (float)(i0 + t)) * c;
-    }
-    __syncthreads();
-    const int k = t;
-    float acc = 0.f;
-    for (int ii = 0; ii < 64; ++ii) {
-        int i = i0 + ii;
-        if (i < realN)
-            acc = fmaf(wc[ii], src[(size_t)(realN - 1 - i) * DK + k], acc);
-    }
-    float wlev;
-    if (b < NCS)            wlev = 0.2f;
-    else if (b < NCS + NCP) wlev = 0.3f;
-    else                    wlev = (0.5f / 256.0f) * gscal[0];
-    atomicAdd(&out[k], wlev * acc);
 }
 
 extern "C" void kernel_launch(void* const* d_in, const int* in_sizes, int n_in,
@@ -601,10 +598,10 @@
     const float* Wv  = (const float*)d_in[4];
     const float* bv  = (const float*)d_in[5];
 
-    const int T = in_sizes[0] / D_EMB;
-    const int P = T / 5;
-    const int NCS  = (T + 63) / 64;
-    const int NCP  = (P + 63) / 64;
+    int T = in_sizes[0] / D_EMB;
+    int P = T / 5;
+    int NCS  = (T + 63) / 64;
+    int NCP  = (P + 63) / 64;
     const int PADS = NCS * 64;
     const int PADP = NCP * 64;
     const int NCH  = NCS + 2 * NCP;
@@ -625,12 +622,14 @@
     float* BPB2  = BPB1  + PADP;
     float* gscal = BPB2  + PADP;
 
-    prep_kernel<<<(T / 4) * 2 + 1, 256, 0, stream>>>(emb, Wk, bk, Wv, bv,
-                                                     K, V, USrev, (float*)d_out, T);
-    graminv_kernel<<<NCH, 256, 0, stream>>>(K, V, USrev, UPrev, UPfwd,
-                                            PV, SVv, AinvT, F1, biasF, P, NCS, NCP);
-    solve_kernel<<<2, 512, 0, stream>>>(USrev, UPrev, UPfwd, AinvT, F1, biasF, q,
-                                        BS, BPB1, BPB2, gscal, NCS, NCP);
-    accum_kernel<<<NCH, 256, 0, stream>>>(V, PV, AinvT, BS, BPB1, BPB2, gscal,
-                                          (float*)d_out, T, P, NCS, NCP);
+    float* out = (float*)d_out;
+
+    void* args[] = {
+        (void*)&emb, (void*)&q, (void*)&Wk, (void*)&bk, (void*)&Wv, (void*)&bv,
+        (void*)&K, (void*)&V, (void*)&PV, (void*)&USrev, (void*)&UPrev, (void*)&UPfwd,
+        (void*)&SVv, (void*)&AinvT, (void*)&F1, (void*)&biasF, (void*)&BS, (void*)&BPB1,
+        (void*)&BPB2, (void*)&gscal, (void*)&out, (void*)&T, (void*)&P, (void*)&NCS, (void*)&NCP
+    };
+    hipLaunchCooperativeKernel(reinterpret_cast<void*>(mega_kernel),
+                               dim3(256), dim3(256), args, 0, stream);
 }
```

After: 298.1 us. +60.3%, slower.
